# Optimization experiments

Hardware: AMD Instinct MI355X
Metric: run time of the kernel (lower is better)

## Reference

```python
import jax, jax.numpy as jnp
import numpy as np

B, NPER, K = 32, 256, 32
N, E = B * NPER, B * NPER * 32
H, NF, NG, L = 128, 128, 50, 6
CUTOFF = 10.0
LOG2 = 0.6931471805599453


def _ssp(x):
    # ShiftedSoftplus: softplus(x) - log(2)
    return jax.nn.softplus(x) - LOG2


def setup_inputs() -> dict:
    key = jax.random.key(0)
    ks = jax.random.split(key, 16)
    rng = np.random.default_rng(0)

    pos = jnp.asarray(rng.uniform(0.0, 5.0, size=(N, 3)).astype(np.float32))
    z = jnp.asarray(rng.integers(1, 100, size=(N,)).astype(np.int32))
    batch = jnp.asarray((np.arange(N) // NPER).astype(np.int32))
    # K neighbors per atom, within the same graph, no self-loops; dst sorted
    dst = np.repeat(np.arange(N), K)
    off = rng.integers(1, NPER, size=N * K)
    src = (dst % NPER + off) % NPER + (dst // NPER) * NPER
    edge_index = jnp.asarray(np.stack([src, dst]).astype(np.int32))
    domain_ids = jnp.asarray(rng.integers(0, 5, size=(B,)).astype(np.int32))

    def dense(k, i, o):
        return jax.random.normal(k, (i, o), jnp.float32) / np.sqrt(i)

    def stackw(k, i, o):
        return jax.random.normal(k, (L, i, o), jnp.float32) / np.sqrt(i)

    return {
        'pos': pos, 'z': z, 'batch': batch, 'edge_index': edge_index,
        'domain_ids': domain_ids,
        'embedding': jax.random.normal(ks[0], (100, H), jnp.float32),
        'mlp_w1': stackw(ks[1], NG, NF), 'mlp_b1': jnp.zeros((L, NF), jnp.float32),
        'mlp_w2': stackw(ks[2], NF, NF), 'mlp_b2': jnp.zeros((L, NF), jnp.float32),
        'cf_lin1_w': stackw(ks[3], H, NF),
        'cf_lin2_w': stackw(ks[4], NF, H), 'cf_lin2_b': jnp.zeros((L, H), jnp.float32),
        'int_lin_w': stackw(ks[5], H, H), 'int_lin_b': jnp.zeros((L, H), jnp.float32),
        'out_w1': dense(ks[6], H, H // 2), 'out_b1': jnp.zeros((H // 2,), jnp.float32),
        'out_w2': dense(ks[7], H // 2, 1), 'out_b2': jnp.zeros((1,), jnp.float32),
        'dom_emb': jax.random.normal(ks[8], (5, 64), jnp.float32),
        'film_w1': dense(ks[9], 64, 128), 'film_b1': jnp.zeros((128,), jnp.float32),
        'film_w2': dense(ks[10], 128, 128), 'film_b2': jnp.zeros((128,), jnp.float32),
        'gamma_w': dense(ks[11], 128, H), 'gamma_b': jnp.zeros((H,), jnp.float32),
        'beta_w': dense(ks[12], 128, H), 'beta_b': jnp.zeros((H,), jnp.float32),
    }


def reference(pos, z, batch, edge_index, domain_ids, embedding,
              mlp_w1, mlp_b1, mlp_w2, mlp_b2, cf_lin1_w, cf_lin2_w, cf_lin2_b,
              int_lin_w, int_lin_b, out_w1, out_b1, out_w2, out_b2,
              dom_emb, film_w1, film_b1, film_w2, film_b2,
              gamma_w, gamma_b, beta_w, beta_b):
    n_atoms = pos.shape[0]
    n_graphs = domain_ids.shape[0]
    src, dst = edge_index[0], edge_index[1]

    # edge distances, gaussian smearing, cosine cutoff (computed once)
    d = jnp.sqrt(jnp.sum((pos[src] - pos[dst]) ** 2, axis=-1))          # [E]
    offsets = jnp.linspace(0.0, CUTOFF, NG).astype(pos.dtype)
    coeff = -0.5 / (CUTOFF / (NG - 1)) ** 2
    edge_attr = jnp.exp(coeff * (d[:, None] - offsets) ** 2)            # [E,NG]
    C = 0.5 * (jnp.cos(d * (np.pi / CUTOFF)) + 1.0)                     # [E]

    h = embedding[z]                                                    # [N,H]
    for l in range(L):
        # filter network on gaussian basis, modulated by cosine cutoff
        W = (_ssp(edge_attr @ mlp_w1[l] + mlp_b1[l]) @ mlp_w2[l] + mlp_b2[l]) * C[:, None]  # [E,NF]
        x = h @ cf_lin1_w[l]                                            # [N,NF]
        msg = x[src] * W                                                # [E,NF]
        agg = jax.ops.segment_sum(msg, dst, num_segments=n_atoms)       # [N,NF]
        x = agg @ cf_lin2_w[l] + cf_lin2_b[l]                           # [N,H]
        h = h + _ssp(x) @ int_lin_w[l] + int_lin_b[l]                   # residual

    atom_e = _ssp(h @ out_w1 + out_b1) @ out_w2 + out_b2                # [N,1]
    e_graph = jax.ops.segment_sum(atom_e, batch, num_segments=n_graphs) # [B,1]

    # FiLM domain bias (features are zeros, so gamma path contributes 0 - faithful)
    de = dom_emb[domain_ids]                                            # [B,64]
    film = jax.nn.relu(de @ film_w1 + film_b1) @ film_w2 + film_b2      # [B,128]
    gamma = film @ gamma_w + gamma_b                                    # [B,H]
    beta = film @ beta_w + beta_b                                       # [B,H]
    dummy = jnp.zeros((n_graphs, H), pos.dtype)
    bias = jnp.sum(gamma * dummy + beta, axis=-1)                       # [B]

    # faithful broadcast [B,1]+[B] -> [B,B], then sum(dim=1) as in original
    energy = jnp.sum(e_graph + bias[None, :], axis=1)                   # [B]

    forces = jnp.zeros((n_atoms, 3), energy.dtype)
    stress = jnp.zeros((n_graphs, 3, 3), energy.dtype)
    features = jnp.zeros((n_atoms, H), energy.dtype)
    return energy, forces, stress, features
```

## Files before the change

kernel.cpp:

```cpp
#include <hip/hip_runtime.h>
#include <math.h>

using uint = unsigned int;
typedef _Float16 h2    __attribute__((ext_vector_type(2)));
typedef _Float16 f16x8 __attribute__((ext_vector_type(8)));
typedef float    f32x4 __attribute__((ext_vector_type(4)));

#define N_ATOMS 8192
#define NEDGE   262144
#define KNBR    32
#define NGAUSS  50
#define NLAYER  6
#define NB      32
#define GTAB    2048
#define DMAX    8.6603f
#define FCUT    10.0f
#define MB      1048576

#define NSETUP  512

#define LSTRIDE 76
#define S_WT    0
#define S_AS    9728

#define WA_OFF  0
#define WB_OFF  8192
#define AS_OFF  16384
#define TS_OFF  17408
#define LAY_N   18432

#define T_W1    0
#define T_W2    4096
#define T_RBF   12288
#define T_HID   13312
#define TAB_SMEM 15360

#define OW1P_OFF 147456
#define PACK_END 151552
#define X_STR    524288

__device__ __forceinline__ float ssp(float x) {
    return fmaxf(x, 0.0f) + log1pf(expf(-fabsf(x))) - 0.69314718055994531f;
}
__device__ __forceinline__ uint pack2(float a, float b) {
    union { h2 h; uint u; } x;
    h2 v; v.x = (_Float16)a; v.y = (_Float16)b; x.h = v; return x.u;
}
__device__ __forceinline__ h2 u2h(uint u) {
    union { uint u; h2 h; } x; x.u = u; return x.h;
}
__device__ __forceinline__ uint h2u(h2 h) {
    union { h2 h; uint u; } x; x.h = h; return x.u;
}
__device__ __forceinline__ float fdot2f(h2 a, h2 b, float c) {
#if __has_builtin(__builtin_amdgcn_fdot2)
    return __builtin_amdgcn_fdot2(a, b, c, false);
#else
    return fmaf((float)a.y, (float)b.y, fmaf((float)a.x, (float)b.x, c));
#endif
}

__device__ __forceinline__ int swz(int row, int quad) {
    return row * 64 + ((quad ^ (row & 15)) << 2);
}
__device__ __forceinline__ int swzc(int row, int c) {
    return row * 64 + (((c >> 2) ^ (row & 15)) << 2) + (c & 3);
}

__device__ __forceinline__ void stage_sw(uint* dst, const uint* __restrict__ src,
                                         int n16, int tid) {
    for (int i = tid; i < n16; i += 256) {
        uint4 v = ((const uint4*)src)[i];
        *(uint4*)&dst[swz(i >> 4, i & 15)] = v;
    }
}

template<int NCT>
__device__ __forceinline__ void run_gemm_sw(const uint* smA, const uint* smW,
                                            int lane, int nb, f32x4* acc) {
    int m = lane & 15, q = lane >> 4;
    #pragma unroll
    for (int ks = 0; ks < 4; ++ks) {
        int cq = q + ks * 4;
        f16x8 a = *(const f16x8*)&smA[swz(m, cq)];
        #pragma unroll
        for (int ct = 0; ct < NCT; ++ct) {
            int n = nb + ct * 16 + m;
            f16x8 b = *(const f16x8*)&smW[swz(n, cq)];
            acc[ct] = __builtin_amdgcn_mfma_f32_16x16x32_f16(a, b, acc[ct], 0, 0, 0);
        }
    }
}

template<int NCT>
__device__ __forceinline__ void run_gemm(const uint* sm, int as_off, int lane,
                                         int nb, f32x4* acc) {
    int m = lane & 15, q = lane >> 4;
    #pragma unroll
    for (int ks = 0; ks < 4; ++ks) {
        f16x8 a = *(const f16x8*)&sm[as_off + m * LSTRIDE + q * 4 + ks * 16];
        #pragma unroll
        for (int ct = 0; ct < NCT; ++ct) {
            f16x8 b = *(const f16x8*)&sm[S_WT + (nb + ct * 16 + m) * LSTRIDE + q * 4 + ks * 16];
            acc[ct] = __builtin_amdgcn_mfma_f32_16x16x32_f16(a, b, acc[ct], 0, 0, 0);
        }
    }
}

struct SArgs {
    const float *pos; const int *z; const int *ei; const int *dom;
    const float *emb;
    const float *cf1; const float *cf2w; const float *intw; const float *ow1;
    const float *dome; const float *fw1; const float *fb1;
    const float *fw2; const float *fb2; const float *bw; const float *bb;
    uint *epack; float *h; uint *xA;
    float *gbias; uint *wpack; uint *bar;
    float *out; int out_size;
};

__global__ void __launch_bounds__(256) k_setup(SArgs a) {
    __shared__ __align__(16) uint sm[S_AS + 1216];
    const int tid = threadIdx.x, bid = blockIdx.x;
    const int gidx = bid * 256 + tid, gsz = NSETUP * 256;
    const int lane = tid & 63, w = tid >> 6;
    const int m = lane & 15, q = lane >> 4;
    const int rowbase = bid * 16;

    for (int i = gidx; i < a.out_size; i += gsz) a.out[i] = 0.0f;
    if (gidx < 256) a.bar[gidx] = 0u;

    for (int idx = gidx; idx < PACK_END; idx += gsz) {
        if (idx < OW1P_OFF) {
            int mat = idx >> 13, e = idx & 8191;
            int kp = e >> 7, cc = e & 127;
            const float* src = (mat < 6) ? (a.cf1 + mat * 16384)
                            : (mat < 12) ? (a.cf2w + (mat - 6) * 16384)
                                         : (a.intw + (mat - 12) * 16384);
            a.wpack[mat * 8192 + cc * 64 + kp] =
                pack2(src[2 * kp * 128 + cc], src[(2 * kp + 1) * 128 + cc]);
        } else {
            int e = idx - OW1P_OFF;
            int kp = e >> 6, cc = e & 63;
            a.wpack[OW1P_OFF + cc * 64 + kp] =
                pack2(a.ow1[2 * kp * 64 + cc], a.ow1[(2 * kp + 1) * 64 + cc]);
        }
    }

    const float invdelta = (float)(GTAB - 1) / DMAX;
    #pragma unroll
    for (int t = 0; t < 2; ++t) {
        int e = rowbase * KNBR + t * 256 + tid;
        int s = a.ei[e], d = a.ei[NEDGE + e];
        float dx = a.pos[3*s] - a.pos[3*d];
        float dy = a.pos[3*s+1] - a.pos[3*d+1];
        float dz = a.pos[3*s+2] - a.pos[3*d+2];
        float dist = sqrtf(dx*dx + dy*dy + dz*dz);
        float u = dist * invdelta;
        int i0 = (int)(u + 0.5f); i0 = (i0 < GTAB - 1) ? i0 : (GTAB - 1);
        a.epack[e] = (uint)s | ((uint)i0 << 16);
    }

    for (int i = tid; i < 1024; i += 256) {
        int r = i >> 6, f2 = i & 63;
        int zz = a.z[rowbase + r];
        float2 v = *(const float2*)&a.emb[zz * 128 + f2 * 2];
        *(float2*)&a.h[(rowbase + r) * 128 + f2 * 2] = v;
        sm[S_AS + r * LSTRIDE + f2] = pack2(v.x, v.y);
    }
    for (int i = tid; i < 2048; i += 256) {
        int m4 = i >> 7, cc = i & 127;
        float v[8];
        #pragma unroll
        for (int j = 0; j < 8; ++j) v[j] = a.cf1[(8 * m4 + j) * 128 + cc];
        uint4 pk; pk.x = pack2(v[0], v[1]); pk.y = pack2(v[2], v[3]);
        pk.z = pack2(v[4], v[5]); pk.w = pack2(v[6], v[7]);
        *(uint4*)&sm[cc * LSTRIDE + m4 * 4] = pk;
    }
    __syncthreads();
    {
        f32x4 acc[2] = {{0,0,0,0},{0,0,0,0}};
        run_gemm<2>(sm, S_AS, lane, w * 32, acc);
        #pragma unroll
        for (int ct = 0; ct < 2; ++ct) {
            int n = w * 32 + ct * 16 + m;
            #pragma unroll
            for (int i = 0; i < 4; ++i) {
                float v = acc[ct][i];
                float u = __shfl_xor(v, 1, 64);
                if (!(lane & 1))
                    a.xA[(rowbase + q * 4 + i) * 64 + (n >> 1)] = pack2(v, u);
            }
        }
    }
    __syncthreads();
    if (bid >= 32 && bid < 64) {
        int g = bid - 32;
        float* fs = (float*)sm;
        if (tid < 64) fs[tid] = a.dome[a.dom[g] * 64 + tid];
        __syncthreads();
        if (tid < 128) {
            float acc = a.fb1[tid];
            for (int i = 0; i < 64; ++i) acc = fmaf(fs[i], a.fw1[i*128 + tid], acc);
            fs[64 + tid] = fmaxf(acc, 0.0f);
        }
        __syncthreads();
        if (tid < 128) {
            float acc = a.fb2[tid];
            for (int i = 0; i < 128; ++i) acc = fmaf(fs[64+i], a.fw2[i*128 + tid], acc);
            fs[192 + tid] = acc;
        }
        __syncthreads();
        if (tid < 128) {
            float acc = a.bb[tid];
            for (int i = 0; i < 128; ++i) acc = fmaf(fs[192+i], a.bw[i*128 + tid], acc);
            #pragma unroll
            for (int off = 32; off > 0; off >>= 1) acc += __shfl_down(acc, off, 64);
            if ((tid & 63) == 0) fs[320 + (tid >> 6)] = acc;
        }
        __syncthreads();
        if (tid == 0) a.gbias[g] = fs[320] + fs[321];
    }
}

__global__ void __launch_bounds__(256) k_table(
    const float* __restrict__ mw1, const float* __restrict__ mb1,
    const float* __restrict__ mw2, const float* __restrict__ mb2,
    uint* __restrict__ tab) {
    __shared__ __align__(16) uint sm[TAB_SMEM];
    const int tid = threadIdx.x;
    const int l = blockIdx.x >> 6;
    const int base = (blockIdx.x & 63) * 32;
    for (int i = tid; i < 4096; i += 256) {
        int kp = i >> 7, cc = i & 127, g0 = 2 * kp;
        float va = (g0 < NGAUSS)     ? mw1[l*NGAUSS*128 + g0*128 + cc]     : 0.f;
        float vb = (g0 + 1 < NGAUSS) ? mw1[l*NGAUSS*128 + (g0+1)*128 + cc] : 0.f;
        sm[T_W1 + i] = pack2(va, vb);
    }
    for (int i = tid; i < 8192; i += 256) {
        int kp = i >> 7, cc = i & 127;
        sm[T_W2 + i] = pack2(mw2[l*16384 + 2*kp*128 + cc],
                             mw2[l*16384 + (2*kp+1)*128 + cc]);
    }
    const float delta = DMAX / (float)(GTAB - 1);
    const float gstep = FCUT / (float)(NGAUSS - 1);
    const float coeff = -0.5f / (gstep * gstep);
    for (int i = tid; i < 1024; i += 256) {
        int r = i >> 5, kp = i & 31;
        float dv = (float)(base + r) * delta;
        int g0 = 2 * kp;
        float v0 = 0.f, v1 = 0.f;
        if (g0 < NGAUSS)     { float t = dv - (float)g0 * gstep;     v0 = expf(coeff*t*t); }
        if (g0 + 1 < NGAUSS) { float t = dv - (float)(g0+1) * gstep; v1 = expf(coeff*t*t); }
        sm[T_RBF + i] = pack2(v0, v1);
    }
    __syncthreads();
    int tx = tid & 31, ty = tid >> 5, c0 = tx * 4, tr0 = ty * 4;
    float acc[4][4];
    #pragma unroll
    for (int i = 0; i < 4; ++i) { acc[i][0]=0.f; acc[i][1]=0.f; acc[i][2]=0.f; acc[i][3]=0.f; }
    #pragma unroll
    for (int oct = 0; oct < 8; ++oct) {
        int kp0 = oct * 4;
        uint4 w_[4];
        #pragma unroll
        for (int p = 0; p < 4; ++p) w_[p] = *(const uint4*)&sm[T_W1 + (kp0+p)*128 + c0];
        #pragma unroll
        for (int i = 0; i < 4; ++i) {
            uint4 av = *(const uint4*)&sm[T_RBF + (tr0+i)*32 + kp0];
            uint aa[4] = {av.x, av.y, av.z, av.w};
            #pragma unroll
            for (int p = 0; p < 4; ++p) {
                h2 ap = u2h(aa[p]);
                acc[i][0] = fdot2f(ap, u2h(w_[p].x), acc[i][0]);
                acc[i][1] = fdot2f(ap, u2h(w_[p].y), acc[i][1]);
                acc[i][2] = fdot2f(ap, u2h(w_[p].z), acc[i][2]);
                acc[i][3] = fdot2f(ap, u2h(w_[p].w), acc[i][3]);
            }
        }
    }
    float4 b1v = *(const float4*)&mb1[l*128 + c0];
    #pragma unroll
    for (int i = 0; i < 4; ++i) {
        uint2 o;
        o.x = pack2(ssp(acc[i][0] + b1v.x), ssp(acc[i][1] + b1v.y));
        o.y = pack2(ssp(acc[i][2] + b1v.z), ssp(acc[i][3] + b1v.w));
        *(uint2*)&sm[T_HID + (tr0+i)*64 + (c0 >> 1)] = o;
    }
    __syncthreads();
    float acc2[4][4];
    #pragma unroll
    for (int i = 0; i < 4; ++i) { acc2[i][0]=0.f; acc2[i][1]=0.f; acc2[i][2]=0.f; acc2[i][3]=0.f; }
    #pragma unroll 4
    for (int oct = 0; oct < 16; ++oct) {
        int kp0 = oct * 4;
        uint4 w_[4];
        #pragma unroll
        for (int p = 0; p < 4; ++p) w_[p] = *(const uint4*)&sm[T_W2 + (kp0+p)*128 + c0];
        #pragma unroll
        for (int i = 0; i < 4; ++i) {
            uint4 av = *(const uint4*)&sm[T_HID + (tr0+i)*64 + kp0];
            uint aa[4] = {av.x, av.y, av.z, av.w};
            #pragma unroll
            for (int p = 0; p < 4; ++p) {
                h2 ap = u2h(aa[p]);
                acc2[i][0] = fdot2f(ap, u2h(w_[p].x), acc2[i][0]);
                acc2[i][1] = fdot2f(ap, u2h(w_[p].y), acc2[i][1]);
                acc2[i][2] = fdot2f(ap, u2h(w_[p].z), acc2[i][2]);
                acc2[i][3] = fdot2f(ap, u2h(w_[p].w), acc2[i][3]);
            }
        }
    }
    float4 b2v = *(const float4*)&mb2[l*128 + c0];
    #pragma unroll
    for (int i = 0; i < 4; ++i) {
        int row = base + tr0 + i;
        float dv = (float)row * delta;
        float Cd = 0.5f * (cosf(dv * 0.3141592653589793f) + 1.0f);
        uint2 o;
        o.x = pack2((acc2[i][0] + b2v.x)*Cd, (acc2[i][1] + b2v.y)*Cd);
        o.y = pack2((acc2[i][2] + b2v.z)*Cd, (acc2[i][3] + b2v.w)*Cd);
        *(uint2*)&tab[(l*GTAB + row)*64 + tx*2] = o;
    }
}

struct LArgs {
    const float* h;
    const uint* x0;
    uint* xb;
    const uint* tab;
    const uint* epack;
    const uint* wpack;
    const float* cf2b;
    const float* intb;
    const float* ob1; const float* ow2; const float* ob2;
    const float* gbias;
    float* out;
    uint* bar;
};

__global__ void __launch_bounds__(256, 2) k_fused(LArgs a) {
    __shared__ __align__(16) uint sm[LAY_N];
    const int tid = threadIdx.x, bid = blockIdx.x;
    const int lane = tid & 63, w = tid >> 6;
    const int m = lane & 15, q = lane >> 4;
    const int xcd = bid & 7;
    const int j   = bid >> 3;
    const int g   = xcd * 4 + (j >> 4);
    const int sub = j & 15;
    const int rowbase = g * 256 + sub * 16;

    float hr[2][4];
    #pragma unroll
    for (int ct = 0; ct < 2; ++ct)
        #pragma unroll
        for (int i = 0; i < 4; ++i)
            hr[ct][i] = a.h[(rowbase + q * 4 + i) * 128 + w * 32 + ct * 16 + m];

    const uint* xr = a.x0;
    uint* xw = a.xb;

    #pragma unroll 1
    for (int l = 0; l < NLAYER; ++l) {
        const bool last = (l == NLAYER - 1);
        const uint* w2p  = a.wpack + (6 + l) * 8192;
        const uint* w3p  = a.wpack + (12 + l) * 8192;
        const uint* w1np = last ? (a.wpack + OW1P_OFF) : (a.wpack + (l + 1) * 8192);
        const uint* tabl = a.tab + l * (GTAB * 64);
        const float* b2 = a.cf2b + l * 128;
        const float* b3 = a.intb + l * 128;

        stage_sw(&sm[WA_OFF], w2p, 2048, tid);
        {
            const int side = lane >> 5, l5 = lane & 31;
            #pragma unroll
            for (int p = 0; p < 4; ++p) {
                int al = p * 4 + w;
                uint ep = a.epack[(rowbase + al) * KNBR + l5];
                h2 a0; a0.x = (_Float16)0; a0.y = (_Float16)0;
                h2 a1 = a0;
                #pragma unroll 4
                for (int k = 0; k < 16; ++k) {
                    uint v = __shfl(ep, 2 * k + side, 64);
                    uint2 tv = *(const uint2*)&tabl[(v >> 16) * 64 + l5 * 2];
                    uint2 xv = *(const uint2*)&xr[(v & 0xffffu) * 64 + l5 * 2];
                    a0 = a0 + u2h(xv.x) * u2h(tv.x);
                    a1 = a1 + u2h(xv.y) * u2h(tv.y);
                }
                uint u0 = h2u(a0), u1 = h2u(a1);
                uint p0 = __shfl_xor(u0, 32, 64), p1 = __shfl_xor(u1, 32, 64);
                if (side == 0) {
                    h2 r0 = u2h(u0) + u2h(p0), r1 = u2h(u1) + u2h(p1);
                    uint2 o; o.x = h2u(r0); o.y = h2u(r1);
                    *(uint2*)&sm[AS_OFF + swzc(al, l5 * 2)] = o;
                }
            }
        }
        __syncthreads();
        stage_sw(&sm[WB_OFF], w3p, 2048, tid);
        {
            f32x4 acc[2] = {{0,0,0,0},{0,0,0,0}};
            run_gemm_sw<2>(&sm[AS_OFF], &sm[WA_OFF], lane, w * 32, acc);
            #pragma unroll
            for (int ct = 0; ct < 2; ++ct) {
                int n = w * 32 + ct * 16 + m;
                float bv = b2[n];
                #pragma unroll
                for (int i = 0; i < 4; ++i) {
                    float v = ssp(acc[ct][i] + bv);
                    float u = __shfl_xor(v, 1, 64);
                    if (!(lane & 1))
                        sm[TS_OFF + swzc(q * 4 + i, n >> 1)] = pack2(v, u);
                }
            }
        }
        __syncthreads();
        stage_sw(&sm[WA_OFF], w1np, last ? 1024 : 2048, tid);
        {
            f32x4 acc[2] = {{0,0,0,0},{0,0,0,0}};
            run_gemm_sw<2>(&sm[TS_OFF], &sm[WB_OFF], lane, w * 32, acc);
            #pragma unroll
            for (int ct = 0; ct < 2; ++ct) {
                int n = w * 32 + ct * 16 + m;
                float bv = b3[n];
                #pragma unroll
                for (int i = 0; i < 4; ++i) {
                    float hv = hr[ct][i] + acc[ct][i] + bv;
                    hr[ct][i] = hv;
                    float u = __shfl_xor(hv, 1, 64);
                    if (!(lane & 1))
                        sm[AS_OFF + swzc(q * 4 + i, n >> 1)] = pack2(hv, u);
                }
            }
        }
        __syncthreads();
        if (!last) {
            f32x4 acc[2] = {{0,0,0,0},{0,0,0,0}};
            run_gemm_sw<2>(&sm[AS_OFF], &sm[WA_OFF], lane, w * 32, acc);
            #pragma unroll
            for (int ct = 0; ct < 2; ++ct) {
                int n = w * 32 + ct * 16 + m;
                #pragma unroll
                for (int i = 0; i < 4; ++i) {
                    float v = acc[ct][i];
                    float u = __shfl_xor(v, 1, 64);
                    if (!(lane & 1))
                        xw[(rowbase + q * 4 + i) * 64 + (n >> 1)] = pack2(v, u);
                }
            }
            __syncthreads();
            if (tid == 0) {
                uint* c = a.bar + l * NB + g;
                __hip_atomic_fetch_add(c, 1u, __ATOMIC_RELAXED,
                                       __HIP_MEMORY_SCOPE_AGENT);
                int it = 0;
                while (__hip_atomic_load(c, __ATOMIC_RELAXED,
                                         __HIP_MEMORY_SCOPE_AGENT) < 16u
                       && ++it < (1 << 19))
                    __builtin_amdgcn_s_sleep(1);
            }
            __syncthreads();
            xr = xw; xw += X_STR;
        } else {
            f32x4 acc[1] = {{0,0,0,0}};
            run_gemm_sw<1>(&sm[AS_OFF], &sm[WA_OFF], lane, w * 16, acc);
            int n = w * 16 + m;
            float b1v = a.ob1[n], w2v = a.ow2[n];
            float part = 0.f;
            #pragma unroll
            for (int i = 0; i < 4; ++i) part += ssp(acc[0][i] + b1v) * w2v;
            #pragma unroll
            for (int mm = 1; mm < 64; mm <<= 1) part += __shfl_xor(part, mm, 64);
            float* fs = (float*)&sm[TS_OFF];
            if (lane == 0) fs[w] = part;
            __syncthreads();
            if (tid == 0) {
                float bsum = fs[0] + fs[1] + fs[2] + fs[3] + 16.0f * a.ob2[0];
                float add = 32.0f * bsum;
                if (sub == 0) {
                    float sb = 0.f;
                    for (int jj = 0; jj < NB; ++jj) sb += a.gbias[jj];
                    add += sb;
                }
                atomicAdd(&a.out[g], add);
            }
        }
    }
}

extern "C" void kernel_launch(void* const* d_in, const int* in_sizes, int n_in,
                              void* d_out, int out_size, void* d_ws, size_t ws_size,
                              hipStream_t stream) {
    SArgs a;
    a.pos  = (const float*)d_in[0];
    a.z    = (const int*)d_in[1];
    a.ei   = (const int*)d_in[3];
    a.dom  = (const int*)d_in[4];
    a.emb  = (const float*)d_in[5];
    const float* mw1 = (const float*)d_in[6];
    const float* mb1 = (const float*)d_in[7];
    const float* mw2 = (const float*)d_in[8];
    const float* mb2 = (const float*)d_in[9];
    a.cf1  = (const float*)d_in[10];
    a.cf2w = (const float*)d_in[11];
    const float* cf2b = (const float*)d_in[12];
    a.intw = (const float*)d_in[13];
    const float* intb = (const float*)d_in[14];
    a.ow1  = (const float*)d_in[15];
    const float* ob1  = (const float*)d_in[16];
    const float* ow2  = (const float*)d_in[17];
    const float* ob2  = (const float*)d_in[18];
    a.dome = (const float*)d_in[19];
    a.fw1  = (const float*)d_in[20];
    a.fb1  = (const float*)d_in[21];
    a.fw2  = (const float*)d_in[22];
    a.fb2  = (const float*)d_in[23];
    a.bw   = (const float*)d_in[26];
    a.bb   = (const float*)d_in[27];

    char* ws = (char*)d_ws;
    a.epack   = (uint*)(ws + 0);
    uint* tab = (uint*)(ws + 2*MB);
    a.h       = (float*)(ws + 5*MB);
    a.xA      = (uint*)(ws + 9*MB);
    uint* xb  = (uint*)(ws + 11*MB);
    a.gbias   = (float*)(ws + 21*MB);
    a.bar     = (uint*)(ws + 21*MB + 4096);
    a.wpack   = (uint*)(ws + 21*MB + 8192);
    a.out = (float*)d_out;
    a.out_size = out_size;

    k_setup<<<NSETUP, 256, 0, stream>>>(a);
    k_table<<<384, 256, 0, stream>>>(mw1, mb1, mw2, mb2, tab);

    LArgs la;
    la.h = a.h; la.x0 = a.xA; la.xb = xb;
    la.tab = tab; la.epack = a.epack; la.wpack = a.wpack;
    la.cf2b = cf2b; la.intb = intb;
    la.ob1 = ob1; la.ow2 = ow2; la.ob2 = ob2;
    la.gbias = a.gbias; la.out = (float*)d_out; la.bar = a.bar;

    k_fused<<<dim3(512), dim3(256), 0, stream>>>(la);
}
```

Before: 275.6 us.

## Fuse setup, filter-table and layer kernels into one persistent kernel

```diff
diff --git a/kernel.cpp b/kernel.cpp
--- a/kernel.cpp
+++ b/kernel.cpp
@@ -17,12 +17,6 @@
 #define FCUT    10.0f
 #define MB      1048576
 
-#define NSETUP  512
-
-#define LSTRIDE 76
-#define S_WT    0
-#define S_AS    9728
-
 #define WA_OFF  0
 #define WB_OFF  8192
 #define AS_OFF  16384
@@ -33,11 +27,12 @@
 #define T_W2    4096
 #define T_RBF   12288
 #define T_HID   13312
-#define TAB_SMEM 15360
 
 #define OW1P_OFF 147456
 #define PACK_END 151552
 #define X_STR    524288
+
+#define GBAR    512
 
 __device__ __forceinline__ float ssp(float x) {
     return fmaxf(x, 0.0f) + log1pf(expf(-fabsf(x))) - 0.69314718055994531f;
@@ -92,42 +87,33 @@
     }
 }
 
-template<int NCT>
-__device__ __forceinline__ void run_gemm(const uint* sm, int as_off, int lane,
-                                         int nb, f32x4* acc) {
-    int m = lane & 15, q = lane >> 4;
-    #pragma unroll
-    for (int ks = 0; ks < 4; ++ks) {
-        f16x8 a = *(const f16x8*)&sm[as_off + m * LSTRIDE + q * 4 + ks * 16];
-        #pragma unroll
-        for (int ct = 0; ct < NCT; ++ct) {
-            f16x8 b = *(const f16x8*)&sm[S_WT + (nb + ct * 16 + m) * LSTRIDE + q * 4 + ks * 16];
-            acc[ct] = __builtin_amdgcn_mfma_f32_16x16x32_f16(a, b, acc[ct], 0, 0, 0);
-        }
-    }
-}
-
-struct SArgs {
+struct AArgs {
     const float *pos; const int *z; const int *ei; const int *dom;
     const float *emb;
     const float *cf1; const float *cf2w; const float *intw; const float *ow1;
+    const float *mw1; const float *mb1; const float *mw2; const float *mb2;
     const float *dome; const float *fw1; const float *fb1;
     const float *fw2; const float *fb2; const float *bw; const float *bb;
-    uint *epack; float *h; uint *xA;
+    const float *cf2b; const float *intb;
+    const float *ob1; const float *ow2; const float *ob2;
+    uint *epack; uint *xA; uint *xb; uint *tab;
     float *gbias; uint *wpack; uint *bar;
     float *out; int out_size;
 };
 
-__global__ void __launch_bounds__(256) k_setup(SArgs a) {
-    __shared__ __align__(16) uint sm[S_AS + 1216];
+__global__ void __launch_bounds__(256, 2) k_all(AArgs a) {
+    __shared__ __align__(16) uint sm[LAY_N];
     const int tid = threadIdx.x, bid = blockIdx.x;
-    const int gidx = bid * 256 + tid, gsz = NSETUP * 256;
+    const int gidx = bid * 256 + tid, gsz = 512 * 256;
     const int lane = tid & 63, w = tid >> 6;
     const int m = lane & 15, q = lane >> 4;
-    const int rowbase = bid * 16;
+    const int xcd = bid & 7;
+    const int j   = bid >> 3;
+    const int g   = xcd * 4 + (j >> 4);
+    const int sub = j & 15;
+    const int rowbase = g * 256 + sub * 16;
 
     for (int i = gidx; i < a.out_size; i += gsz) a.out[i] = 0.0f;
-    if (gidx < 256) a.bar[gidx] = 0u;
 
     for (int idx = gidx; idx < PACK_END; idx += gsz) {
         if (idx < OW1P_OFF) {
@@ -160,26 +146,168 @@
         a.epack[e] = (uint)s | ((uint)i0 << 16);
     }
 
-    for (int i = tid; i < 1024; i += 256) {
-        int r = i >> 6, f2 = i & 63;
-        int zz = a.z[rowbase + r];
-        float2 v = *(const float2*)&a.emb[zz * 128 + f2 * 2];
-        *(float2*)&a.h[(rowbase + r) * 128 + f2 * 2] = v;
-        sm[S_AS + r * LSTRIDE + f2] = pack2(v.x, v.y);
-    }
-    for (int i = tid; i < 2048; i += 256) {
-        int m4 = i >> 7, cc = i & 127;
-        float v[8];
-        #pragma unroll
-        for (int j = 0; j < 8; ++j) v[j] = a.cf1[(8 * m4 + j) * 128 + cc];
-        uint4 pk; pk.x = pack2(v[0], v[1]); pk.y = pack2(v[2], v[3]);
-        pk.z = pack2(v[4], v[5]); pk.w = pack2(v[6], v[7]);
-        *(uint4*)&sm[cc * LSTRIDE + m4 * 4] = pk;
+    float hr[2][4];
+    #pragma unroll
+    for (int i = 0; i < 4; ++i) {
+        int zz = a.z[rowbase + q * 4 + i];
+        #pragma unroll
+        for (int ct = 0; ct < 2; ++ct)
+            hr[ct][i] = a.emb[zz * 128 + w * 32 + ct * 16 + m];
+    }
+
+    if (sub == 0) {
+        float* fs = (float*)sm;
+        if (tid < 64) fs[tid] = a.dome[a.dom[g] * 64 + tid];
+        __syncthreads();
+        if (tid < 128) {
+            float acc = a.fb1[tid];
+            for (int i = 0; i < 64; ++i) acc = fmaf(fs[i], a.fw1[i*128 + tid], acc);
+            fs[64 + tid] = fmaxf(acc, 0.0f);
+        }
+        __syncthreads();
+        if (tid < 128) {
+            float acc = a.fb2[tid];
+            for (int i = 0; i < 128; ++i) acc = fmaf(fs[64+i], a.fw2[i*128 + tid], acc);
+            fs[192 + tid] = acc;
+        }
+        __syncthreads();
+        if (tid < 128) {
+            float acc = a.bb[tid];
+            for (int i = 0; i < 128; ++i) acc = fmaf(fs[192+i], a.bw[i*128 + tid], acc);
+            #pragma unroll
+            for (int off = 32; off > 0; off >>= 1) acc += __shfl_down(acc, off, 64);
+            if ((tid & 63) == 0) fs[320 + (tid >> 6)] = acc;
+        }
+        __syncthreads();
+        if (tid == 0) a.gbias[g] = fs[320] + fs[321];
+        __syncthreads();
+    }
+
+    if (bid < 384) {
+        const int tl = bid >> 6;
+        const int base = (bid & 63) * 32;
+        for (int i = tid; i < 4096; i += 256) {
+            int kp = i >> 7, cc = i & 127, g0 = 2 * kp;
+            float va = (g0 < NGAUSS)     ? a.mw1[tl*NGAUSS*128 + g0*128 + cc]     : 0.f;
+            float vb = (g0 + 1 < NGAUSS) ? a.mw1[tl*NGAUSS*128 + (g0+1)*128 + cc] : 0.f;
+            sm[T_W1 + i] = pack2(va, vb);
+        }
+        for (int i = tid; i < 8192; i += 256) {
+            int kp = i >> 7, cc = i & 127;
+            sm[T_W2 + i] = pack2(a.mw2[tl*16384 + 2*kp*128 + cc],
+                                 a.mw2[tl*16384 + (2*kp+1)*128 + cc]);
+        }
+        const float delta = DMAX / (float)(GTAB - 1);
+        const float gstep = FCUT / (float)(NGAUSS - 1);
+        const float coeff = -0.5f / (gstep * gstep);
+        for (int i = tid; i < 1024; i += 256) {
+            int r = i >> 5, kp = i & 31;
+            float dv = (float)(base + r) * delta;
+            int g0 = 2 * kp;
+            float v0 = 0.f, v1 = 0.f;
+            if (g0 < NGAUSS)     { float t = dv - (float)g0 * gstep;     v0 = expf(coeff*t*t); }
+            if (g0 + 1 < NGAUSS) { float t = dv - (float)(g0+1) * gstep; v1 = expf(coeff*t*t); }
+            sm[T_RBF + i] = pack2(v0, v1);
+        }
+        __syncthreads();
+        int tx = tid & 31, ty = tid >> 5, c0 = tx * 4, tr0 = ty * 4;
+        float acc[4][4];
+        #pragma unroll
+        for (int i = 0; i < 4; ++i) { acc[i][0]=0.f; acc[i][1]=0.f; acc[i][2]=0.f; acc[i][3]=0.f; }
+        #pragma unroll
+        for (int oct = 0; oct < 8; ++oct) {
+            int kp0 = oct * 4;
+            uint4 w_[4];
+            #pragma unroll
+            for (int p = 0; p < 4; ++p) w_[p] = *(const uint4*)&sm[T_W1 + (kp0+p)*128 + c0];
+            #pragma unroll
+            for (int i = 0; i < 4; ++i) {
+                uint4 av = *(const uint4*)&sm[T_RBF + (tr0+i)*32 + kp0];
+                uint aa[4] = {av.x, av.y, av.z, av.w};
+                #pragma unroll
+                for (int p = 0; p < 4; ++p) {
+                    h2 ap = u2h(aa[p]);
+                    acc[i][0] = fdot2f(ap, u2h(w_[p].x), acc[i][0]);
+                    acc[i][1] = fdot2f(ap, u2h(w_[p].y), acc[i][1]);
+                    acc[i][2] = fdot2f(ap, u2h(w_[p].z), acc[i][2]);
+                    acc[i][3] = fdot2f(ap, u2h(w_[p].w), acc[i][3]);
+                }
+            }
+        }
+        float4 b1v = *(const float4*)&a.mb1[tl*128 + c0];
+        #pragma unroll
+        for (int i = 0; i < 4; ++i) {
+            uint2 o;
+            o.x = pack2(ssp(acc[i][0] + b1v.x), ssp(acc[i][1] + b1v.y));
+            o.y = pack2(ssp(acc[i][2] + b1v.z), ssp(acc[i][3] + b1v.w));
+            *(uint2*)&sm[T_HID + (tr0+i)*64 + (c0 >> 1)] = o;
+        }
+        __syncthreads();
+        float acc2[4][4];
+        #pragma unroll
+        for (int i = 0; i < 4; ++i) { acc2[i][0]=0.f; acc2[i][1]=0.f; acc2[i][2]=0.f; acc2[i][3]=0.f; }
+        #pragma unroll 4
+        for (int oct = 0; oct < 16; ++oct) {
+            int kp0 = oct * 4;
+            uint4 w_[4];
+            #pragma unroll
+            for (int p = 0; p < 4; ++p) w_[p] = *(const uint4*)&sm[T_W2 + (kp0+p)*128 + c0];
+            #pragma unroll
+            for (int i = 0; i < 4; ++i) {
+                uint4 av = *(const uint4*)&sm[T_HID + (tr0+i)*64 + kp0];
+                uint aa[4] = {av.x, av.y, av.z, av.w};
+                #pragma unroll
+                for (int p = 0; p < 4; ++p) {
+                    h2 ap = u2h(aa[p]);
+                    acc2[i][0] = fdot2f(ap, u2h(w_[p].x), acc2[i][0]);
+                    acc2[i][1] = fdot2f(ap, u2h(w_[p].y), acc2[i][1]);
+                    acc2[i][2] = fdot2f(ap, u2h(w_[p].z), acc2[i][2]);
+                    acc2[i][3] = fdot2f(ap, u2h(w_[p].w), acc2[i][3]);
+                }
+            }
+        }
+        float4 b2v = *(const float4*)&a.mb2[tl*128 + c0];
+        #pragma unroll
+        for (int i = 0; i < 4; ++i) {
+            int row = base + tr0 + i;
+            float dv = (float)row * delta;
+            float Cd = 0.5f * (cosf(dv * 0.3141592653589793f) + 1.0f);
+            uint2 o;
+            o.x = pack2((acc2[i][0] + b2v.x)*Cd, (acc2[i][1] + b2v.y)*Cd);
+            o.y = pack2((acc2[i][2] + b2v.z)*Cd, (acc2[i][3] + b2v.w)*Cd);
+            *(uint2*)&a.tab[(tl*GTAB + row)*64 + tx*2] = o;
+        }
+    }
+
+    __syncthreads();
+    if (tid == 0) {
+        __hip_atomic_fetch_add(&a.bar[GBAR], 1u, __ATOMIC_RELEASE,
+                               __HIP_MEMORY_SCOPE_AGENT);
+        int it = 0;
+        while (__hip_atomic_load(&a.bar[GBAR], __ATOMIC_RELAXED,
+                                 __HIP_MEMORY_SCOPE_AGENT) < 512u
+               && ++it < (1 << 21))
+            __builtin_amdgcn_s_sleep(2);
+        __builtin_amdgcn_fence(__ATOMIC_ACQUIRE, "agent");
+    }
+    __syncthreads();
+
+    stage_sw(&sm[WA_OFF], a.wpack, 2048, tid);
+    #pragma unroll
+    for (int ct = 0; ct < 2; ++ct) {
+        int n = w * 32 + ct * 16 + m;
+        #pragma unroll
+        for (int i = 0; i < 4; ++i) {
+            float hv = hr[ct][i];
+            float u = __shfl_xor(hv, 1, 64);
+            if (!(lane & 1))
+                sm[AS_OFF + swzc(q * 4 + i, n >> 1)] = pack2(hv, u);
+        }
     }
     __syncthreads();
     {
         f32x4 acc[2] = {{0,0,0,0},{0,0,0,0}};
-        run_gemm<2>(sm, S_AS, lane, w * 32, acc);
+        run_gemm_sw<2>(&sm[AS_OFF], &sm[WA_OFF], lane, w * 32, acc);
         #pragma unroll
         for (int ct = 0; ct < 2; ++ct) {
             int n = w * 32 + ct * 16 + m;
@@ -193,170 +321,17 @@
         }
     }
     __syncthreads();
-    if (bid >= 32 && bid < 64) {
-        int g = bid - 32;
-        float* fs = (float*)sm;
-        if (tid < 64) fs[tid] = a.dome[a.dom[g] * 64 + tid];
-        __syncthreads();
-        if (tid < 128) {
-            float acc = a.fb1[tid];
-            for (int i = 0; i < 64; ++i) acc = fmaf(fs[i], a.fw1[i*128 + tid], acc);
-            fs[64 + tid] = fmaxf(acc, 0.0f);
-        }
-        __syncthreads();
-        if (tid < 128) {
-            float acc = a.fb2[tid];
-            for (int i = 0; i < 128; ++i) acc = fmaf(fs[64+i], a.fw2[i*128 + tid], acc);
-            fs[192 + tid] = acc;
-        }
-        __syncthreads();
-        if (tid < 128) {
-            float acc = a.bb[tid];
-            for (int i = 0; i < 128; ++i) acc = fmaf(fs[192+i], a.bw[i*128 + tid], acc);
-            #pragma unroll
-            for (int off = 32; off > 0; off >>= 1) acc += __shfl_down(acc, off, 64);
-            if ((tid & 63) == 0) fs[320 + (tid >> 6)] = acc;
-        }
-        __syncthreads();
-        if (tid == 0) a.gbias[g] = fs[320] + fs[321];
-    }
-}
-
-__global__ void __launch_bounds__(256) k_table(
-    const float* __restrict__ mw1, const float* __restrict__ mb1,
-    const float* __restrict__ mw2, const float* __restrict__ mb2,
-    uint* __restrict__ tab) {
-    __shared__ __align__(16) uint sm[TAB_SMEM];
-    const int tid = threadIdx.x;
-    const int l = blockIdx.x >> 6;
-    const int base = (blockIdx.x & 63) * 32;
-    for (int i = tid; i < 4096; i += 256) {
-        int kp = i >> 7, cc = i & 127, g0 = 2 * kp;
-        float va = (g0 < NGAUSS)     ? mw1[l*NGAUSS*128 + g0*128 + cc]     : 0.f;
-        float vb = (g0 + 1 < NGAUSS) ? mw1[l*NGAUSS*128 + (g0+1)*128 + cc] : 0.f;
-        sm[T_W1 + i] = pack2(va, vb);
-    }
-    for (int i = tid; i < 8192; i += 256) {
-        int kp = i >> 7, cc = i & 127;
-        sm[T_W2 + i] = pack2(mw2[l*16384 + 2*kp*128 + cc],
-                             mw2[l*16384 + (2*kp+1)*128 + cc]);
-    }
-    const float delta = DMAX / (float)(GTAB - 1);
-    const float gstep = FCUT / (float)(NGAUSS - 1);
-    const float coeff = -0.5f / (gstep * gstep);
-    for (int i = tid; i < 1024; i += 256) {
-        int r = i >> 5, kp = i & 31;
-        float dv = (float)(base + r) * delta;
-        int g0 = 2 * kp;
-        float v0 = 0.f, v1 = 0.f;
-        if (g0 < NGAUSS)     { float t = dv - (float)g0 * gstep;     v0 = expf(coeff*t*t); }
-        if (g0 + 1 < NGAUSS) { float t = dv - (float)(g0+1) * gstep; v1 = expf(coeff*t*t); }
-        sm[T_RBF + i] = pack2(v0, v1);
+    if (tid == 0) {
+        uint* c = a.bar + g;
+        __hip_atomic_fetch_add(c, 1u, __ATOMIC_RELAXED, __HIP_MEMORY_SCOPE_AGENT);
+        int it = 0;
+        while (__hip_atomic_load(c, __ATOMIC_RELAXED, __HIP_MEMORY_SCOPE_AGENT) < 16u
+               && ++it < (1 << 19))
+            __builtin_amdgcn_s_sleep(1);
     }
     __syncthreads();
-    int tx = tid & 31, ty = tid >> 5, c0 = tx * 4, tr0 = ty * 4;
-    float acc[4][4];
-    #pragma unroll
-    for (int i = 0; i < 4; ++i) { acc[i][0]=0.f; acc[i][1]=0.f; acc[i][2]=0.f; acc[i][3]=0.f; }
-    #pragma unroll
-    for (int oct = 0; oct < 8; ++oct) {
-        int kp0 = oct * 4;
-        uint4 w_[4];
-        #pragma unroll
-        for (int p = 0; p < 4; ++p) w_[p] = *(const uint4*)&sm[T_W1 + (kp0+p)*128 + c0];
-        #pragma unroll
-        for (int i = 0; i < 4; ++i) {
-            uint4 av = *(const uint4*)&sm[T_RBF + (tr0+i)*32 + kp0];
-            uint aa[4] = {av.x, av.y, av.z, av.w};
-            #pragma unroll
-            for (int p = 0; p < 4; ++p) {
-                h2 ap = u2h(aa[p]);
-                acc[i][0] = fdot2f(ap, u2h(w_[p].x), acc[i][0]);
-                acc[i][1] = fdot2f(ap, u2h(w_[p].y), acc[i][1]);
-                acc[i][2] = fdot2f(ap, u2h(w_[p].z), acc[i][2]);
-                acc[i][3] = fdot2f(ap, u2h(w_[p].w), acc[i][3]);
-            }
-        }
-    }
-    float4 b1v = *(const float4*)&mb1[l*128 + c0];
-    #pragma unroll
-    for (int i = 0; i < 4; ++i) {
-        uint2 o;
-        o.x = pack2(ssp(acc[i][0] + b1v.x), ssp(acc[i][1] + b1v.y));
-        o.y = pack2(ssp(acc[i][2] + b1v.z), ssp(acc[i][3] + b1v.w));
-        *(uint2*)&sm[T_HID + (tr0+i)*64 + (c0 >> 1)] = o;
-    }
-    __syncthreads();
-    float acc2[4][4];
-    #pragma unroll
-    for (int i = 0; i < 4; ++i) { acc2[i][0]=0.f; acc2[i][1]=0.f; acc2[i][2]=0.f; acc2[i][3]=0.f; }
-    #pragma unroll 4
-    for (int oct = 0; oct < 16; ++oct) {
-        int kp0 = oct * 4;
-        uint4 w_[4];
-        #pragma unroll
-        for (int p = 0; p < 4; ++p) w_[p] = *(const uint4*)&sm[T_W2 + (kp0+p)*128 + c0];
-        #pragma unroll
-        for (int i = 0; i < 4; ++i) {
-            uint4 av = *(const uint4*)&sm[T_HID + (tr0+i)*64 + kp0];
-            uint aa[4] = {av.x, av.y, av.z, av.w};
-            #pragma unroll
-            for (int p = 0; p < 4; ++p) {
-                h2 ap = u2h(aa[p]);
-                acc2[i][0] = fdot2f(ap, u2h(w_[p].x), acc2[i][0]);
-                acc2[i][1] = fdot2f(ap, u2h(w_[p].y), acc2[i][1]);
-                acc2[i][2] = fdot2f(ap, u2h(w_[p].z), acc2[i][2]);
-                acc2[i][3] = fdot2f(ap, u2h(w_[p].w), acc2[i][3]);
-            }
-        }
-    }
-    float4 b2v = *(const float4*)&mb2[l*128 + c0];
-    #pragma unroll
-    for (int i = 0; i < 4; ++i) {
-        int row = base + tr0 + i;
-        float dv = (float)row * delta;
-        float Cd = 0.5f * (cosf(dv * 0.3141592653589793f) + 1.0f);
-        uint2 o;
-        o.x = pack2((acc2[i][0] + b2v.x)*Cd, (acc2[i][1] + b2v.y)*Cd);
-        o.y = pack2((acc2[i][2] + b2v.z)*Cd, (acc2[i][3] + b2v.w)*Cd);
-        *(uint2*)&tab[(l*GTAB + row)*64 + tx*2] = o;
-    }
-}
-
-struct LArgs {
-    const float* h;
-    const uint* x0;
-    uint* xb;
-    const uint* tab;
-    const uint* epack;
-    const uint* wpack;
-    const float* cf2b;
-    const float* intb;
-    const float* ob1; const float* ow2; const float* ob2;
-    const float* gbias;
-    float* out;
-    uint* bar;
-};
-
-__global__ void __launch_bounds__(256, 2) k_fused(LArgs a) {
-    __shared__ __align__(16) uint sm[LAY_N];
-    const int tid = threadIdx.x, bid = blockIdx.x;
-    const int lane = tid & 63, w = tid >> 6;
-    const int m = lane & 15, q = lane >> 4;
-    const int xcd = bid & 7;
-    const int j   = bid >> 3;
-    const int g   = xcd * 4 + (j >> 4);
-    const int sub = j & 15;
-    const int rowbase = g * 256 + sub * 16;
-
-    float hr[2][4];
-    #pragma unroll
-    for (int ct = 0; ct < 2; ++ct)
-        #pragma unroll
-        for (int i = 0; i < 4; ++i)
-            hr[ct][i] = a.h[(rowbase + q * 4 + i) * 128 + w * 32 + ct * 16 + m];
-
-    const uint* xr = a.x0;
+
+    const uint* xr = a.xA;
     uint* xw = a.xb;
 
     #pragma unroll 1
@@ -449,7 +424,7 @@
             }
             __syncthreads();
             if (tid == 0) {
-                uint* c = a.bar + l * NB + g;
+                uint* c = a.bar + NB + l * NB + g;
                 __hip_atomic_fetch_add(c, 1u, __ATOMIC_RELAXED,
                                        __HIP_MEMORY_SCOPE_AGENT);
                 int it = 0;
@@ -490,25 +465,25 @@
 extern "C" void kernel_launch(void* const* d_in, const int* in_sizes, int n_in,
                               void* d_out, int out_size, void* d_ws, size_t ws_size,
                               hipStream_t stream) {
-    SArgs a;
+    AArgs a;
     a.pos  = (const float*)d_in[0];
     a.z    = (const int*)d_in[1];
     a.ei   = (const int*)d_in[3];
     a.dom  = (const int*)d_in[4];
     a.emb  = (const float*)d_in[5];
-    const float* mw1 = (const float*)d_in[6];
-    const float* mb1 = (const float*)d_in[7];
-    const float* mw2 = (const float*)d_in[8];
-    const float* mb2 = (const float*)d_in[9];
+    a.mw1  = (const float*)d_in[6];
+    a.mb1  = (const float*)d_in[7];
+    a.mw2  = (const float*)d_in[8];
+    a.mb2  = (const float*)d_in[9];
     a.cf1  = (const float*)d_in[10];
     a.cf2w = (const float*)d_in[11];
-    const float* cf2b = (const float*)d_in[12];
+    a.cf2b = (const float*)d_in[12];
     a.intw = (const float*)d_in[13];
-    const float* intb = (const float*)d_in[14];
+    a.intb = (const float*)d_in[14];
     a.ow1  = (const float*)d_in[15];
-    const float* ob1  = (const float*)d_in[16];
-    const float* ow2  = (const float*)d_in[17];
-    const float* ob2  = (const float*)d_in[18];
+    a.ob1  = (const float*)d_in[16];
+    a.ow2  = (const float*)d_in[17];
+    a.ob2  = (const float*)d_in[18];
     a.dome = (const float*)d_in[19];
     a.fw1  = (const float*)d_in[20];
     a.fb1  = (const float*)d_in[21];
@@ -519,25 +494,15 @@
 
     char* ws = (char*)d_ws;
     a.epack   = (uint*)(ws + 0);
-    uint* tab = (uint*)(ws + 2*MB);
-    a.h       = (float*)(ws + 5*MB);
+    a.tab     = (uint*)(ws + 2*MB);
     a.xA      = (uint*)(ws + 9*MB);
-    uint* xb  = (uint*)(ws + 11*MB);
+    a.xb      = (uint*)(ws + 11*MB);
     a.gbias   = (float*)(ws + 21*MB);
     a.bar     = (uint*)(ws + 21*MB + 4096);
     a.wpack   = (uint*)(ws + 21*MB + 8192);
     a.out = (float*)d_out;
     a.out_size = out_size;
 
-    k_setup<<<NSETUP, 256, 0, stream>>>(a);
-    k_table<<<384, 256, 0, stream>>>(mw1, mb1, mw2, mb2, tab);
-
-    LArgs la;
-    la.h = a.h; la.x0 = a.xA; la.xb = xb;
-    la.tab = tab; la.epack = a.epack; la.wpack = a.wpack;
-    la.cf2b = cf2b; la.intb = intb;
-    la.ob1 = ob1; la.ow2 = ow2; la.ob2 = ob2;
-    la.gbias = a.gbias; la.out = (float*)d_out; la.bar = a.bar;
-
-    k_fused<<<dim3(512), dim3(256), 0, stream>>>(la);
-}
+    hipMemsetAsync(a.bar, 0, 4096, stream);
+    k_all<<<dim3(512), dim3(256), 0, stream>>>(a);
+}
```

Measured after the change: 301.9 us. 9.5% more time.

## Halve rows per block, hold GEMM weights in registers, double grid size

Applied to the files above, without the earlier changes.

```diff
diff --git a/kernel.cpp b/kernel.cpp
--- a/kernel.cpp
+++ b/kernel.cpp
@@ -23,11 +23,9 @@
 #define S_WT    0
 #define S_AS    9728
 
-#define WA_OFF  0
-#define WB_OFF  8192
-#define AS_OFF  16384
-#define TS_OFF  17408
-#define LAY_N   18432
+#define AS_OFF  0
+#define TS_OFF  1024
+#define LAYF_N  2112
 
 #define T_W1    0
 #define T_W2    4096
@@ -67,27 +65,29 @@
     return row * 64 + (((c >> 2) ^ (row & 15)) << 2) + (c & 3);
 }
 
-__device__ __forceinline__ void stage_sw(uint* dst, const uint* __restrict__ src,
-                                         int n16, int tid) {
-    for (int i = tid; i < n16; i += 256) {
-        uint4 v = ((const uint4*)src)[i];
-        *(uint4*)&dst[swz(i >> 4, i & 15)] = v;
-    }
-}
-
 template<int NCT>
-__device__ __forceinline__ void run_gemm_sw(const uint* smA, const uint* smW,
-                                            int lane, int nb, f32x4* acc) {
+__device__ __forceinline__ void load_bf(const uint* __restrict__ wp, int lane,
+                                        uint4* bf) {
     int m = lane & 15, q = lane >> 4;
     #pragma unroll
+    for (int ct = 0; ct < NCT; ++ct)
+        #pragma unroll
+        for (int ks = 0; ks < 4; ++ks)
+            bf[ct * 4 + ks] =
+                *(const uint4*)&wp[(ct * 16 + m) * 64 + (q + ks * 4) * 4];
+}
+
+template<int NCT>
+__device__ __forceinline__ void run_gemm_breg(const uint* smA, const uint4* bf,
+                                              int lane, f32x4* acc) {
+    int m = lane & 15, q = lane >> 4;
+    #pragma unroll
     for (int ks = 0; ks < 4; ++ks) {
-        int cq = q + ks * 4;
-        f16x8 a = *(const f16x8*)&smA[swz(m, cq)];
+        f16x8 a = *(const f16x8*)&smA[swz(m, q + ks * 4)];
         #pragma unroll
         for (int ct = 0; ct < NCT; ++ct) {
-            int n = nb + ct * 16 + m;
-            f16x8 b = *(const f16x8*)&smW[swz(n, cq)];
-            acc[ct] = __builtin_amdgcn_mfma_f32_16x16x32_f16(a, b, acc[ct], 0, 0, 0);
+            union { uint4 u; f16x8 h; } b; b.u = bf[ct * 4 + ks];
+            acc[ct] = __builtin_amdgcn_mfma_f32_16x16x32_f16(a, b.h, acc[ct], 0, 0, 0);
         }
     }
 }
@@ -338,23 +338,26 @@
     uint* bar;
 };
 
-__global__ void __launch_bounds__(256, 2) k_fused(LArgs a) {
-    __shared__ __align__(16) uint sm[LAY_N];
+__global__ void __launch_bounds__(256, 4) k_fused(LArgs a) {
+    __shared__ __align__(16) uint sm[LAYF_N];
     const int tid = threadIdx.x, bid = blockIdx.x;
     const int lane = tid & 63, w = tid >> 6;
     const int m = lane & 15, q = lane >> 4;
     const int xcd = bid & 7;
     const int j   = bid >> 3;
-    const int g   = xcd * 4 + (j >> 4);
-    const int sub = j & 15;
-    const int rowbase = g * 256 + sub * 16;
+    const int g   = xcd * 4 + (j >> 5);
+    const int sub = j & 31;
+    const int rowbase = g * 256 + sub * 8;
 
     float hr[2][4];
     #pragma unroll
     for (int ct = 0; ct < 2; ++ct)
         #pragma unroll
-        for (int i = 0; i < 4; ++i)
-            hr[ct][i] = a.h[(rowbase + q * 4 + i) * 128 + w * 32 + ct * 16 + m];
+        for (int i = 0; i < 4; ++i) {
+            int r = q * 4 + i;
+            hr[ct][i] = (r < 8)
+                ? a.h[(rowbase + r) * 128 + w * 32 + ct * 16 + m] : 0.0f;
+        }
 
     const uint* xr = a.x0;
     uint* xw = a.xb;
@@ -369,11 +372,12 @@
         const float* b2 = a.cf2b + l * 128;
         const float* b3 = a.intb + l * 128;
 
-        stage_sw(&sm[WA_OFF], w2p, 2048, tid);
+        uint4 bf[8];
+        load_bf<2>(w2p + (w * 32) * 64, lane, bf);
         {
             const int side = lane >> 5, l5 = lane & 31;
             #pragma unroll
-            for (int p = 0; p < 4; ++p) {
+            for (int p = 0; p < 2; ++p) {
                 int al = p * 4 + w;
                 uint ep = a.epack[(rowbase + al) * KNBR + l5];
                 h2 a0; a0.x = (_Float16)0; a0.y = (_Float16)0;
@@ -396,10 +400,9 @@
             }
         }
         __syncthreads();
-        stage_sw(&sm[WB_OFF], w3p, 2048, tid);
         {
             f32x4 acc[2] = {{0,0,0,0},{0,0,0,0}};
-            run_gemm_sw<2>(&sm[AS_OFF], &sm[WA_OFF], lane, w * 32, acc);
+            run_gemm_breg<2>(&sm[AS_OFF], bf, lane, acc);
             #pragma unroll
             for (int ct = 0; ct < 2; ++ct) {
                 int n = w * 32 + ct * 16 + m;
@@ -413,11 +416,11 @@
                 }
             }
         }
-        __syncthreads();
-        stage_sw(&sm[WA_OFF], w1np, last ? 1024 : 2048, tid);
+        load_bf<2>(w3p + (w * 32) * 64, lane, bf);
+        __syncthreads();
         {
             f32x4 acc[2] = {{0,0,0,0},{0,0,0,0}};
-            run_gemm_sw<2>(&sm[TS_OFF], &sm[WB_OFF], lane, w * 32, acc);
+            run_gemm_breg<2>(&sm[TS_OFF], bf, lane, acc);
             #pragma unroll
             for (int ct = 0; ct < 2; ++ct) {
                 int n = w * 32 + ct * 16 + m;
@@ -432,10 +435,12 @@
                 }
             }
         }
+        if (last) load_bf<1>(w1np + (w * 16) * 64, lane, bf);
+        else      load_bf<2>(w1np + (w * 32) * 64, lane, bf);
         __syncthreads();
         if (!last) {
             f32x4 acc[2] = {{0,0,0,0},{0,0,0,0}};
-            run_gemm_sw<2>(&sm[AS_OFF], &sm[WA_OFF], lane, w * 32, acc);
+            run_gemm_breg<2>(&sm[AS_OFF], bf, lane, acc);
             #pragma unroll
             for (int ct = 0; ct < 2; ++ct) {
                 int n = w * 32 + ct * 16 + m;
@@ -443,7 +448,7 @@
                 for (int i = 0; i < 4; ++i) {
                     float v = acc[ct][i];
                     float u = __shfl_xor(v, 1, 64);
-                    if (!(lane & 1))
+                    if (!(lane & 1) && (q * 4 + i) < 8)
                         xw[(rowbase + q * 4 + i) * 64 + (n >> 1)] = pack2(v, u);
                 }
             }
@@ -454,7 +459,7 @@
                                        __HIP_MEMORY_SCOPE_AGENT);
                 int it = 0;
                 while (__hip_atomic_load(c, __ATOMIC_RELAXED,
-                                         __HIP_MEMORY_SCOPE_AGENT) < 16u
+                                         __HIP_MEMORY_SCOPE_AGENT) < 32u
                        && ++it < (1 << 19))
                     __builtin_amdgcn_s_sleep(1);
             }
@@ -462,19 +467,20 @@
             xr = xw; xw += X_STR;
         } else {
             f32x4 acc[1] = {{0,0,0,0}};
-            run_gemm_sw<1>(&sm[AS_OFF], &sm[WA_OFF], lane, w * 16, acc);
+            run_gemm_breg<1>(&sm[AS_OFF], bf, lane, acc);
             int n = w * 16 + m;
             float b1v = a.ob1[n], w2v = a.ow2[n];
             float part = 0.f;
             #pragma unroll
-            for (int i = 0; i < 4; ++i) part += ssp(acc[0][i] + b1v) * w2v;
+            for (int i = 0; i < 4; ++i)
+                if (q * 4 + i < 8) part += ssp(acc[0][i] + b1v) * w2v;
             #pragma unroll
             for (int mm = 1; mm < 64; mm <<= 1) part += __shfl_xor(part, mm, 64);
             float* fs = (float*)&sm[TS_OFF];
             if (lane == 0) fs[w] = part;
             __syncthreads();
             if (tid == 0) {
-                float bsum = fs[0] + fs[1] + fs[2] + fs[3] + 16.0f * a.ob2[0];
+                float bsum = fs[0] + fs[1] + fs[2] + fs[3] + 8.0f * a.ob2[0];
                 float add = 32.0f * bsum;
                 if (sub == 0) {
                     float sb = 0.f;
@@ -539,5 +545,5 @@
     la.ob1 = ob1; la.ow2 = ow2; la.ob2 = ob2;
     la.gbias = a.gbias; la.out = (float*)d_out; la.bar = a.bar;
 
-    k_fused<<<dim3(512), dim3(256), 0, stream>>>(la);
-}
+    k_fused<<<dim3(1024), dim3(256), 0, stream>>>(la);
+}
```

After: 557.2 us. 102% more time.
